# Kernel optimization log

Hardware: AMD Instinct MI355X
Metric: run time of the kernel (lower is better)

The kernel has to match this reference:

```python
import jax, jax.numpy as jnp
import numpy as np

WIN = 9
EPS = 1e-05


def _box3d(x, win=WIN):
    """Sum over a win^3 box (zero-padded), equivalent to conv3d with a ones kernel.
    Implemented as three separable 1D convolutions (exact same math, O(win)/voxel)."""
    pad = win // 2
    for axis in range(3):  # spatial axes D, H, W
        kshape = [1, 1, 1, 1, 1]
        kshape[2 + axis] = win
        kern = jnp.ones(kshape, x.dtype)
        pads = [(0, 0)] * 3
        pads[axis] = (pad, pad)
        dn = jax.lax.conv_dimension_numbers(x.shape, kern.shape, ('NCDHW', 'OIDHW', 'NCDHW'))
        x = jax.lax.conv_general_dilated(x, kern, window_strides=(1, 1, 1),
                                         padding=pads, dimension_numbers=dn)
    return x


def setup_inputs() -> dict:
    key = jax.random.key(0)
    k1, k2 = jax.random.split(key)
    shape = (1, 1, 160, 192, 224)  # [N, C, D, H, W] brain-MRI-scale volume
    I = jax.random.normal(k1, shape, dtype=jnp.float32)
    J = jax.random.normal(k2, shape, dtype=jnp.float32)
    return {"I": I, "J": J}


def reference(I, J):
    win_size = WIN ** 3
    I2 = I * I
    J2 = J * J
    IJ = I * J
    I_sum = _box3d(I)
    J_sum = _box3d(J)
    I2_sum = _box3d(I2)
    J2_sum = _box3d(J2)
    IJ_sum = _box3d(IJ)
    u_I = I_sum / win_size
    u_J = J_sum / win_size
    cross = IJ_sum - u_J * I_sum - u_I * J_sum + u_I * u_J * win_size
    I_var = I2_sum - 2 * u_I * I_sum + u_I * u_I * win_size
    J_var = J2_sum - 2 * u_J * J_sum + u_J * u_J * win_size
    cc = cross * cross / (I_var * J_var + EPS)
    return -1.0 * jnp.mean(cc)
```

## Files before the change

kernel.cpp:

```cpp
#include <hip/hip_runtime.h>


#define DD 160
#define HH 192
#define WW 224
#define W4 56
#define SLICE (HH * WW)
#define S4 (SLICE / 4)
#define NVOX (DD * SLICE)
#define TW 32
#define TH 16
#define DCH 19
#define ITERS (DCH + 8)
#define NTHR 512
#define SW_RS 36
#define SW_CS (24 * SW_RS)
#define EPS 1e-5f
#define INV_WSUM (1.0f / 729.0f)

__device__ __forceinline__ void bar_lds_only() {
    __asm__ volatile("" ::: "memory");
    __builtin_amdgcn_s_waitcnt(0xC07F);
    __builtin_amdgcn_s_barrier();
    __asm__ volatile("" ::: "memory");
}

__global__ __launch_bounds__(NTHR, 4) void ncc_fused(const float* __restrict__ I,
                                                     const float* __restrict__ J,
                                                     float* __restrict__ out) {
    __shared__ float SW0[5 * SW_CS], SW1[5 * SW_CS];
    __shared__ float SH[TH * TW * 5];
    __shared__ float wred[NTHR / 64];

    const int tid = threadIdx.x;
    const int tx = tid & 31, ty = tid >> 5;
    const int wlo = blockIdx.x * TW;
    const int hlo = blockIdx.y * TH;
    const int dlo = blockIdx.z * DCH;

    const int wr = tid >> 3, wc = tid & 7;
    const int gh = hlo - 4 + wr;
    const bool hok = (gh >= 0) && (gh < HH);
    const int gf0 = (wlo >> 2) - 1 + wc;

    const int ht = tid - 192;
    const int hcol = ht & 31, hch = ht >> 5;

    const float4* Iv = (const float4*)I;
    const float4* Jv = (const float4*)J;

    float pfa[12], pfb[12];

    auto w_load = [&](int z) {
        const bool zok = (z >= 0) && (z < DD) && hok;
        const int rowb = z * S4 + gh * W4;
        #pragma unroll
        for (int k = 0; k < 3; ++k) {
            const int f = gf0 + k;
            float4 a = make_float4(0.f, 0.f, 0.f, 0.f);
            float4 b = make_float4(0.f, 0.f, 0.f, 0.f);
            if (zok && f >= 0 && f < W4) { a = Iv[rowb + f]; b = Jv[rowb + f]; }
            pfa[4*k] = a.x; pfa[4*k+1] = a.y; pfa[4*k+2] = a.z; pfa[4*k+3] = a.w;
            pfb[4*k] = b.x; pfb[4*k+1] = b.y; pfb[4*k+2] = b.z; pfb[4*k+3] = b.w;
        }
    };

    auto w_compute = [&](float* dst) {
        float* wp = dst + wr * SW_RS + 4 * wc;
        #pragma unroll
        for (int ch = 0; ch < 5; ++ch) {
            float v[12];
            #pragma unroll
            for (int k = 0; k < 12; ++k)
                v[k] = (ch == 0) ? pfa[k]
                     : (ch == 1) ? pfb[k]
                     : (ch == 2) ? pfa[k] * pfa[k]
                     : (ch == 3) ? pfb[k] * pfb[k]
                     :             pfa[k] * pfb[k];
            float s = v[0];
            #pragma unroll
            for (int k = 1; k < 9; ++k) s += v[k];
            float4 o;
            o.x = s;
            s += v[9]  - v[0]; o.y = s;
            s += v[10] - v[1]; o.z = s;
            s += v[11] - v[2]; o.w = s;
            *(float4*)(wp + ch * SW_CS) = o;
        }
    };

    float q0[9], q1[9], q2[9], q3[9], q4[9];
    #pragma unroll
    for (int k = 0; k < 9; ++k) { q0[k]=0.f; q1[k]=0.f; q2[k]=0.f; q3[k]=0.f; q4[k]=0.f; }
    float r0=0.f, r1=0.f, r2=0.f, r3=0.f, r4=0.f;
    float acc = 0.f;

    if (tid < 192) {
        w_load(dlo - 4);
        if (dlo >= 4) w_compute(SW0);
        w_load(dlo - 3);
    }
    bar_lds_only();

    #pragma unroll 1
    for (int g = 0; g < 3; ++g) {
        #pragma unroll
        for (int ph = 0; ph < 9; ++ph) {
            const int i = 9 * g + ph;
            const int z = dlo - 4 + i;
            const bool val = (z >= 0) && (z < DD);
            const int par = i & 1;
            float* swR = par ? SW1 : SW0;
            float* swW = par ? SW0 : SW1;

            if (tid < 192) {
                if (i < ITERS - 1) {
                    const int zn = z + 1;
                    if (zn >= 0 && zn < DD) w_compute(swW);
                    w_load(z + 2);
                }
            } else if (ht < 160 && val) {
                const float* p = swR + hch * SW_CS + hcol;
                float v[24];
                #pragma unroll
                for (int r = 0; r < 24; r += 2) {
                    const float* pr = p + r * SW_RS;
                    v[r]     = pr[0];
                    v[r + 1] = pr[SW_RS];
                }
                float s = v[0];
                #pragma unroll
                for (int r = 1; r < 9; ++r) s += v[r];
                float* o = SH + hcol * 5 + hch;
                float prev = s;
                o[0] = s;
                #pragma unroll
                for (int r = 1; r < 16; ++r) {
                    prev += v[r + 8] - v[r - 1];
                    o[r * (TW * 5)] = prev;
                }
            }
            bar_lds_only();

            float w0=0.f, w1=0.f, w2=0.f, w3=0.f, w4=0.f;
            if (val) {
                const float* p = SH + (ty * TW + tx) * 5;
                w0 = p[0]; w1 = p[1]; w2 = p[2]; w3 = p[3]; w4 = p[4];
            }
            r0 += w0 - q0[ph]; q0[ph] = w0;
            r1 += w1 - q1[ph]; q1[ph] = w1;
            r2 += w2 - q2[ph]; q2[ph] = w2;
            r3 += w3 - q3[ph]; q3[ph] = w3;
            r4 += w4 - q4[ph]; q4[ph] = w4;

            if (i >= 8 && (dlo + i - 8) < DD) {
                float cross = r4 - r0 * r1 * INV_WSUM;
                float iv    = r2 - r0 * r0 * INV_WSUM;
                float jv    = r3 - r1 * r1 * INV_WSUM;
                acc += cross * cross * __builtin_amdgcn_rcpf(iv * jv + EPS);
            }
            bar_lds_only();
        }
    }

    #pragma unroll
    for (int off = 32; off > 0; off >>= 1) acc += __shfl_down(acc, off, 64);
    if ((tid & 63) == 0) wred[tid >> 6] = acc;
    __syncthreads();
    if (tid == 0) {
        float t = 0.f;
        #pragma unroll
        for (int k = 0; k < NTHR / 64; ++k) t += wred[k];
        atomicAdd(out, t * (-1.0f / (float)NVOX));
    }
}

extern "C" void kernel_launch(void* const* d_in, const int* in_sizes, int n_in,
                              void* d_out, int out_size, void* d_ws, size_t ws_size,
                              hipStream_t stream) {
    const float* I = (const float*)d_in[0];
    const float* J = (const float*)d_in[1];
    float* out = (float*)d_out;

    hipMemsetAsync(d_out, 0, sizeof(float), stream);

    dim3 blk(NTHR, 1, 1);
    dim3 grd(WW / TW, HH / TH, (DD + DCH - 1) / DCH);
    ncc_fused<<<grd, blk, 0, stream>>>(I, J, out);
}
```

Baseline: 137.6 us.

## Shrink block to 256 threads, double-buffer H-sum stage, overlap W-stage after read

Halves the tile height to 8 rows and the thread count to 256, and lengthens each block's depth chunk to 28 slices. The W-pass buffer becomes single and the H-pass output is double-buffered instead. The W-pass compute and next load now run after all threads read the H-sums, so work that was split across dedicated warps now runs on shared ones. The aim is higher occupancy and less LDS per block. The cost is a larger halo overhead ratio in H (8 of 16 rows) and a longer serial depth loop per block.

Measured after the change: 127.6 us. -7.3%, faster.

```diff
diff --git a/kernel.cpp b/kernel.cpp
--- a/kernel.cpp
+++ b/kernel.cpp
@@ -9,12 +9,13 @@
 #define S4 (SLICE / 4)
 #define NVOX (DD * SLICE)
 #define TW 32
-#define TH 16
-#define DCH 19
+#define TH 8
+#define DCH 28
 #define ITERS (DCH + 8)
-#define NTHR 512
+#define NTHR 256
 #define SW_RS 36
-#define SW_CS (24 * SW_RS)
+#define SW_CS (16 * SW_RS)
+#define SH_SZ (TH * TW * 5)
 #define EPS 1e-5f
 #define INV_WSUM (1.0f / 729.0f)
 
@@ -28,8 +29,8 @@
 __global__ __launch_bounds__(NTHR, 4) void ncc_fused(const float* __restrict__ I,
                                                      const float* __restrict__ J,
                                                      float* __restrict__ out) {
-    __shared__ float SW0[5 * SW_CS], SW1[5 * SW_CS];
-    __shared__ float SH[TH * TW * 5];
+    __shared__ float SW[5 * SW_CS];
+    __shared__ float SH0[SH_SZ], SH1[SH_SZ];
     __shared__ float wred[NTHR / 64];
 
     const int tid = threadIdx.x;
@@ -38,13 +39,13 @@
     const int hlo = blockIdx.y * TH;
     const int dlo = blockIdx.z * DCH;
 
-    const int wr = tid >> 3, wc = tid & 7;
+    const int wid = tid - 128;
+    const int wr = wid >> 3, wc = wid & 7;
     const int gh = hlo - 4 + wr;
     const bool hok = (gh >= 0) && (gh < HH);
     const int gf0 = (wlo >> 2) - 1 + wc;
 
-    const int ht = tid - 192;
-    const int hcol = ht & 31, hch = ht >> 5;
+    const int hcol = tid & 31, hch = tid >> 5;
 
     const float4* Iv = (const float4*)I;
     const float4* Jv = (const float4*)J;
@@ -65,8 +66,8 @@
         }
     };
 
-    auto w_compute = [&](float* dst) {
-        float* wp = dst + wr * SW_RS + 4 * wc;
+    auto w_compute = [&]() {
+        float* wp = SW + wr * SW_RS + 4 * wc;
         #pragma unroll
         for (int ch = 0; ch < 5; ++ch) {
             float v[12];
@@ -95,35 +96,27 @@
     float r0=0.f, r1=0.f, r2=0.f, r3=0.f, r4=0.f;
     float acc = 0.f;
 
-    if (tid < 192) {
+    if (tid >= 128) {
         w_load(dlo - 4);
-        if (dlo >= 4) w_compute(SW0);
+        if (dlo >= 4) w_compute();
         w_load(dlo - 3);
     }
     bar_lds_only();
 
     #pragma unroll 1
-    for (int g = 0; g < 3; ++g) {
+    for (int g = 0; g < 4; ++g) {
         #pragma unroll
         for (int ph = 0; ph < 9; ++ph) {
             const int i = 9 * g + ph;
             const int z = dlo - 4 + i;
             const bool val = (z >= 0) && (z < DD);
-            const int par = i & 1;
-            float* swR = par ? SW1 : SW0;
-            float* swW = par ? SW0 : SW1;
+            float* shW = (i & 1) ? SH1 : SH0;
 
-            if (tid < 192) {
-                if (i < ITERS - 1) {
-                    const int zn = z + 1;
-                    if (zn >= 0 && zn < DD) w_compute(swW);
-                    w_load(z + 2);
-                }
-            } else if (ht < 160 && val) {
-                const float* p = swR + hch * SW_CS + hcol;
-                float v[24];
+            if (tid < 160 && val) {
+                const float* p = SW + hch * SW_CS + hcol;
+                float v[16];
                 #pragma unroll
-                for (int r = 0; r < 24; r += 2) {
+                for (int r = 0; r < 16; r += 2) {
                     const float* pr = p + r * SW_RS;
                     v[r]     = pr[0];
                     v[r + 1] = pr[SW_RS];
@@ -131,11 +124,11 @@
                 float s = v[0];
                 #pragma unroll
                 for (int r = 1; r < 9; ++r) s += v[r];
-                float* o = SH + hcol * 5 + hch;
+                float* o = shW + hcol * 5 + hch;
                 float prev = s;
                 o[0] = s;
                 #pragma unroll
-                for (int r = 1; r < 16; ++r) {
+                for (int r = 1; r < TH; ++r) {
                     prev += v[r + 8] - v[r - 1];
                     o[r * (TW * 5)] = prev;
                 }
@@ -144,8 +137,13 @@
 
             float w0=0.f, w1=0.f, w2=0.f, w3=0.f, w4=0.f;
             if (val) {
-                const float* p = SH + (ty * TW + tx) * 5;
-                w0 = p[0]; w1 = p[1]; w2 = p[2]; w3 = p[3]; w4 = p[4];
+                const float* pF = shW + (ty * TW + tx) * 5;
+                w0 = pF[0]; w1 = pF[1]; w2 = pF[2]; w3 = pF[3]; w4 = pF[4];
+            }
+            if (tid >= 128 && i < ITERS - 1) {
+                const int zn = z + 1;
+                if (zn >= 0 && zn < DD) w_compute();
+                w_load(z + 2);
             }
             r0 += w0 - q0[ph]; q0[ph] = w0;
             r1 += w1 - q1[ph]; q1[ph] = w1;
```
